# Optimization experiments

Measured on AMD Instinct MI355X. Metric: run time of the kernel, lower is better.

## Reference

```python
import jax, jax.numpy as jnp
import numpy as np

B, T, D, H = 8, 1024, 768, 12
HD = D // H  # 64

def setup_inputs() -> dict:
    key = jax.random.key(0)
    ks = jax.random.split(key, 3)
    x = jax.random.normal(ks[0], (B, T, D), dtype=jnp.float32)
    Wqkv = jax.random.normal(ks[1], (D, 3 * D), dtype=jnp.float32) * (1.0 / np.sqrt(D))
    bqkv = jnp.zeros((3 * D,), dtype=jnp.float32)
    Wproj = jax.random.normal(ks[2], (D, D), dtype=jnp.float32) * (1.0 / np.sqrt(D))
    bproj = jnp.zeros((D,), dtype=jnp.float32)
    return {"x": x, "Wqkv": Wqkv, "bqkv": bqkv, "Wproj": Wproj, "bproj": bproj}

def reference(x, Wqkv, bqkv, Wproj, bproj):
    b, t, d = x.shape
    qkv = x @ Wqkv + bqkv                      # [B,T,3D]
    q, k, v = jnp.split(qkv, 3, axis=-1)
    # [B,T,D] -> [B,H,T,hd]
    q = q.reshape(b, t, H, HD).transpose(0, 2, 1, 3)
    k = k.reshape(b, t, H, HD).transpose(0, 2, 1, 3)
    v = v.reshape(b, t, H, HD).transpose(0, 2, 1, 3)
    scale = 1.0 / np.sqrt(HD)
    att = jnp.einsum('bhqd,bhkd->bhqk', q, k) * scale  # [B,H,T,T]
    causal = jnp.tril(jnp.ones((t, t), dtype=bool))
    att = jnp.where(causal[None, None], att, jnp.float32(-jnp.inf))
    att = jax.nn.softmax(att, axis=-1)
    out = jnp.einsum('bhqk,bhkd->bhqd', att, v)        # [B,H,T,hd]
    out = out.transpose(0, 2, 1, 3).reshape(b, t, d)
    return out @ Wproj + bproj
```

## Files before the change

### kernel.cpp

```cpp
#include <hip/hip_runtime.h>

#define Bn 8
#define Tn 1024
#define Dn 768
#define Hn 12
#define HDn 64
#define D3 (3 * Dn)

typedef float f32x4 __attribute__((ext_vector_type(4)));
typedef short bf16x8 __attribute__((ext_vector_type(8)));
typedef unsigned short u16;

#define SM_SCALE 0.18033688011112042f

__device__ __forceinline__ u16 f2b(float f) {
    unsigned u = __builtin_bit_cast(unsigned, f);
    u += 0x7fffu + ((u >> 16) & 1u);
    return (u16)(u >> 16);
}

__device__ __forceinline__ unsigned cvt_pk_bf16(float lo, float hi) {
    unsigned r;
    asm("v_cvt_pk_bf16_f32 %0, %1, %2" : "=v"(r) : "v"(lo), "v"(hi));
    return r;
}

__device__ __forceinline__ void async_lds16(void* lds, const void* g) {
    __builtin_amdgcn_global_load_lds(
        (const __attribute__((address_space(1))) unsigned int*)g,
        (__attribute__((address_space(3))) unsigned int*)lds, 16, 0, 0);
}

__global__ __launch_bounds__(256)
void conv_bf16_kernel(const float* __restrict__ in, u16* __restrict__ out, int n)
{
    int i = (blockIdx.x * 256 + threadIdx.x) * 4;
    if (i >= n) return;
    float4 v = *(const float4*)&in[i];
    union { u16 u[4]; uint2 p; } r;
    r.u[0] = f2b(v.x); r.u[1] = f2b(v.y); r.u[2] = f2b(v.z); r.u[3] = f2b(v.w);
    *(uint2*)&out[i] = r.p;
}

__global__ __launch_bounds__(256)
void transpose_bf16_kernel(const float* __restrict__ W, u16* __restrict__ WT,
                           int K, int N)
{
    __shared__ float Ls[64][65];
    const int bk = blockIdx.y * 64, bn = blockIdx.x * 64;
    const int r  = threadIdx.x >> 2;
    const int c0 = (threadIdx.x & 3) * 16;
    #pragma unroll
    for (int i = 0; i < 4; ++i) {
        float4 v = *(const float4*)&W[(size_t)(bk + r) * N + bn + c0 + i * 4];
        Ls[r][c0 + i * 4 + 0] = v.x;
        Ls[r][c0 + i * 4 + 1] = v.y;
        Ls[r][c0 + i * 4 + 2] = v.z;
        Ls[r][c0 + i * 4 + 3] = v.w;
    }
    __syncthreads();
    #pragma unroll
    for (int i = 0; i < 16; ++i) {
        WT[(size_t)(bn + r) * K + bk + c0 + i] = f2b(Ls[c0 + i][r]);
    }
}

template <int MODE>
__global__ __launch_bounds__(256)
void gemm_mfma_kernel(const u16* __restrict__ A, const u16* __restrict__ BT,
                      const float* __restrict__ bias, void* __restrict__ Cout,
                      u16* __restrict__ VTout, int M, int N, int K)
{
    __shared__ u16 As[2][128 * 32];
    __shared__ u16 Bs[2][128 * 32];
    const int tid  = threadIdx.x;
    const int w    = tid >> 6;
    const int lane = tid & 63;
    const int li   = lane & 15;
    const int g    = lane >> 4;
    const int wm   = w >> 1, wn = w & 1;

    const int fid = blockIdx.x;
    const int wg  = (fid & 7) * ((int)gridDim.x >> 3) + (fid >> 3);
    const int nbx = N / 128;
    const int bm  = (wg / nbx) * 128;
    const int bn  = (wg % nbx) * 128;

#define GSTAGE(k0s, buf_) do {                                                 \
        _Pragma("unroll")                                                      \
        for (int i_ = 0; i_ < 2; ++i_) {                                       \
            const int L_  = i_ * 256 + tid;                                    \
            const int rp_ = L_ >> 3;                                           \
            const int u_  = (L_ & 7) ^ (rp_ & 7);                              \
            const int row_ = rp_ * 2 + (u_ >> 2);                              \
            const int gc_  = u_ & 3;                                           \
            async_lds16(&As[buf_][(i_ * 256 + w * 64) * 8],                    \
                        &A[(size_t)(bm + row_) * K + (k0s) + gc_ * 8]);        \
            async_lds16(&Bs[buf_][(i_ * 256 + w * 64) * 8],                    \
                        &BT[(size_t)(bn + row_) * K + (k0s) + gc_ * 8]);       \
        }                                                                      \
    } while (0)

    f32x4 acc[4][4];
    #pragma unroll
    for (int i = 0; i < 4; ++i)
        #pragma unroll
        for (int j = 0; j < 4; ++j)
            acc[i][j] = (f32x4){0.f, 0.f, 0.f, 0.f};

    GSTAGE(0, 0);
    __syncthreads();

    const int nk = K / 32;
    for (int kt = 0; kt < nk; ++kt) {
        const int cur = kt & 1;
        if (kt + 1 < nk) GSTAGE((kt + 1) * 32, cur ^ 1);

        bf16x8 af[4], bfr[4];
        #pragma unroll
        for (int fm = 0; fm < 4; ++fm) {
            const int row = wm * 64 + fm * 16 + li;
            const int rp  = row >> 1;
            const int s   = (((row & 1) << 2) | g) ^ (rp & 7);
            af[fm] = *(const bf16x8*)&As[cur][rp * 64 + s * 8];
        }
        #pragma unroll
        for (int fn = 0; fn < 4; ++fn) {
            const int row = wn * 64 + fn * 16 + li;
            const int rp  = row >> 1;
            const int s   = (((row & 1) << 2) | g) ^ (rp & 7);
            bfr[fn] = *(const bf16x8*)&Bs[cur][rp * 64 + s * 8];
        }
        __builtin_amdgcn_s_setprio(1);
        #pragma unroll
        for (int fm = 0; fm < 4; ++fm)
            #pragma unroll
            for (int fn = 0; fn < 4; ++fn)
                acc[fm][fn] = __builtin_amdgcn_mfma_f32_16x16x32_bf16(
                    af[fm], bfr[fn], acc[fm][fn], 0, 0, 0);
        __builtin_amdgcn_s_setprio(0);

        __syncthreads();
    }
#undef GSTAGE

    if (MODE == 1 && bn >= 2 * Dn) {
        #pragma unroll
        for (int fm = 0; fm < 4; ++fm) {
            const int t0g = bm + wm * 64 + fm * 16 + g * 4;
            const int bb = t0g >> 10, tt = t0g & 1023;
            #pragma unroll
            for (int fn = 0; fn < 4; ++fn) {
                const int ncol = bn + wn * 64 + fn * 16 + li;
                const float bs = bias[ncol];
                const int cv = ncol - 2 * Dn;
                const int hv = cv >> 6, dv = cv & 63;
                union { u16 u[4]; uint2 p; } r;
                #pragma unroll
                for (int reg = 0; reg < 4; ++reg)
                    r.u[reg] = f2b(acc[fm][fn][reg] + bs);
                *(uint2*)&VTout[(((size_t)bb * Hn + hv) * HDn + dv) * Tn + tt] = r.p;
            }
        }
    } else {
        #pragma unroll
        for (int fm = 0; fm < 4; ++fm) {
            #pragma unroll
            for (int reg = 0; reg < 4; ++reg) {
                const size_t row = (size_t)(bm + wm * 64 + fm * 16 + g * 4 + reg);
                #pragma unroll
                for (int fn = 0; fn < 4; ++fn) {
                    const int col = bn + wn * 64 + fn * 16 + li;
                    const float v = acc[fm][fn][reg] + bias[col];
                    if (MODE == 1) ((u16*)Cout)[row * N + col] = f2b(v);
                    else           ((float*)Cout)[row * N + col] = v;
                }
            }
        }
    }
}

__global__ __launch_bounds__(256, 3)
void attn_mfma_kernel(const u16* __restrict__ qkvb, const u16* __restrict__ VT,
                      u16* __restrict__ attnb)
{
    __shared__ u16 Ks[2][64 * 64];
    __shared__ u16 Vs[2][64 * 64];
    __shared__ u16 Pb[4][32 * 64];

    const int tid  = threadIdx.x;
    const int w    = tid >> 6;
    const int lane = tid & 63;
    const int li   = lane & 15;
    const int g    = lane >> 4;

    const int fid = blockIdx.x;
    const int xcd = fid & 7, j = fid >> 3;
    const int bh  = xcd + 8 * (j % 12);
    const int qt  = 7 - (j / 12);
    const int b   = bh / 12, h = bh % 12;

    const int q0   = qt * 128;
    const int wrow = q0 + w * 32;
    const size_t rowbase = (size_t)b * Tn;
    const u16* vbase = VT + (size_t)bh * HDn * Tn;
    const u16* kbase = &qkvb[rowbase * D3 + Dn + h * HDn];

#define STAGE(kt_, buf_) do {                                                  \
        const int k0s = (kt_) * 64;                                            \
        _Pragma("unroll")                                                      \
        for (int i_ = 0; i_ < 2; ++i_) {                                       \
            const int L_   = i_ * 256 + tid;                                   \
            const int row_ = L_ >> 3;                                          \
            const int gp_  = (L_ & 7) ^ (row_ & 7);                            \
            async_lds16(&Ks[buf_][(i_ * 256 + w * 64) * 8],                    \
                        &kbase[(size_t)(k0s + row_) * D3 + gp_ * 8]);          \
            async_lds16(&Vs[buf_][(i_ * 256 + w * 64) * 8],                    \
                        &vbase[(size_t)row_ * Tn + k0s + gp_ * 8]);            \
        }                                                                      \
    } while (0)

    STAGE(0, 0);

    bf16x8 qf[2][2];
    #pragma unroll
    for (int rh = 0; rh < 2; ++rh)
        #pragma unroll
        for (int kc = 0; kc < 2; ++kc)
            qf[rh][kc] = *(const bf16x8*)&qkvb[
                (rowbase + wrow + rh * 16 + li) * D3 + h * HDn + kc * 32 + g * 8];

    f32x4 of[2][4];
    float m_run[2], l_run[2];
    #pragma unroll
    for (int rh = 0; rh < 2; ++rh) {
        #pragma unroll
        for (int nf = 0; nf < 4; ++nf) of[rh][nf] = (f32x4){0.f, 0.f, 0.f, 0.f};
        m_run[rh] = -1e30f;
        l_run[rh] = 0.f;
    }

    const int nkt   = (q0 >> 6) + 2;
    const int myend = wrow >> 6;

    __syncthreads();

    for (int kt = 0; kt < nkt; ++kt) {
        const int cur = kt & 1;
        if (kt + 1 < nkt) STAGE(kt + 1, cur ^ 1);

        if (kt <= myend) {
            const int k0 = kt * 64;
            const bool maskit = (kt == myend);

            f32x4 st[2][4];
            #pragma unroll
            for (int rh = 0; rh < 2; ++rh)
                #pragma unroll
                for (int nf = 0; nf < 4; ++nf) st[rh][nf] = (f32x4){0.f, 0.f, 0.f, 0.f};
            __builtin_amdgcn_s_setprio(1);
            #pragma unroll
            for (int kc = 0; kc < 2; ++kc)
                #pragma unroll
                for (int nf = 0; nf < 4; ++nf) {
                    const bf16x8 kf = *(const bf16x8*)&Ks[cur][
                        (nf * 16 + li) * 64 + ((kc * 32 + g * 8) ^ ((li & 7) * 8))];
                    st[0][nf] = __builtin_amdgcn_mfma_f32_16x16x32_bf16(kf, qf[0][kc], st[0][nf], 0, 0, 0);
                    st[1][nf] = __builtin_amdgcn_mfma_f32_16x16x32_bf16(kf, qf[1][kc], st[1][nf], 0, 0, 0);
                }
            __builtin_amdgcn_s_setprio(0);

            #pragma unroll
            for (int rh = 0; rh < 2; ++rh) {
                if (maskit) {
                    const int qg = wrow + rh * 16 + li;
                    #pragma unroll
                    for (int nf = 0; nf < 4; ++nf)
                        #pragma unroll
                        for (int reg = 0; reg < 4; ++reg)
                            if (k0 + nf * 16 + g * 4 + reg > qg) st[rh][nf][reg] = -1e30f;
                }

                float mt = st[rh][0][0];
                #pragma unroll
                for (int nf = 0; nf < 4; ++nf)
                    #pragma unroll
                    for (int reg = 0; reg < 4; ++reg)
                        mt = fmaxf(mt, st[rh][nf][reg]);
                mt = fmaxf(mt, __shfl_xor(mt, 16, 64));
                mt = fmaxf(mt, __shfl_xor(mt, 32, 64));
                const float mts = mt * SM_SCALE;

                const float mold = m_run[rh];
                if (!__all(mts <= mold + 8.0f)) {
                    const float mnew = fmaxf(mold, mts);
                    const float resc = exp2f(mold - mnew);
                    m_run[rh] = mnew;
                    l_run[rh] *= resc;
                    float rs[4];
                    #pragma unroll
                    for (int reg = 0; reg < 4; ++reg)
                        rs[reg] = __shfl(resc, g * 4 + reg, 64);
                    #pragma unroll
                    for (int nf = 0; nf < 4; ++nf)
                        #pragma unroll
                        for (int reg = 0; reg < 4; ++reg)
                            of[rh][nf][reg] *= rs[reg];
                }

                const float mcur = m_run[rh];
                float ls = 0.f;
                u16* pb = &Pb[w][(rh * 16 + li) * 64];
                #pragma unroll
                for (int nf = 0; nf < 4; ++nf) {
                    const float p0 = exp2f(fmaf(st[rh][nf][0], SM_SCALE, -mcur));
                    const float p1 = exp2f(fmaf(st[rh][nf][1], SM_SCALE, -mcur));
                    const float p2 = exp2f(fmaf(st[rh][nf][2], SM_SCALE, -mcur));
                    const float p3 = exp2f(fmaf(st[rh][nf][3], SM_SCALE, -mcur));
                    ls += (p0 + p1) + (p2 + p3);
                    uint2 pk;
                    pk.x = cvt_pk_bf16(p0, p1);
                    pk.y = cvt_pk_bf16(p2, p3);
                    *(uint2*)&pb[(nf * 16 + g * 4) ^ ((li & 7) << 3)] = pk;
                }
                ls += __shfl_xor(ls, 16, 64);
                ls += __shfl_xor(ls, 32, 64);
                l_run[rh] += ls;
            }

            #pragma unroll
            for (int kc = 0; kc < 2; ++kc) {
                const int pcol = (kc * 32 + g * 8) ^ ((li & 7) << 3);
                const bf16x8 pf0 = *(const bf16x8*)&Pb[w][li * 64 + pcol];
                const bf16x8 pf1 = *(const bf16x8*)&Pb[w][(16 + li) * 64 + pcol];
                __builtin_amdgcn_s_setprio(1);
                #pragma unroll
                for (int nf = 0; nf < 4; ++nf) {
                    const bf16x8 vf = *(const bf16x8*)&Vs[cur][
                        (nf * 16 + li) * 64 + ((kc * 32 + g * 8) ^ ((li & 7) * 8))];
                    of[0][nf] = __builtin_amdgcn_mfma_f32_16x16x32_bf16(pf0, vf, of[0][nf], 0, 0, 0);
                    of[1][nf] = __builtin_amdgcn_mfma_f32_16x16x32_bf16(pf1, vf, of[1][nf], 0, 0, 0);
                }
                __builtin_amdgcn_s_setprio(0);
            }
        }

        __syncthreads();
    }
#undef STAGE

    #pragma unroll
    for (int rh = 0; rh < 2; ++rh) {
        const float inv = 1.0f / l_run[rh];
        float rs[4];
        #pragma unroll
        for (int reg = 0; reg < 4; ++reg)
            rs[reg] = __shfl(inv, g * 4 + reg, 64);
        #pragma unroll
        for (int reg = 0; reg < 4; ++reg) {
            const size_t row = rowbase + wrow + rh * 16 + g * 4 + reg;
            #pragma unroll
            for (int nf = 0; nf < 4; ++nf)
                attnb[row * Dn + h * HDn + nf * 16 + li] = f2b(of[rh][nf][reg] * rs[reg]);
        }
    }
}

extern "C" void kernel_launch(void* const* d_in, const int* in_sizes, int n_in,
                              void* d_out, int out_size, void* d_ws, size_t ws_size,
                              hipStream_t stream) {
    const float* x     = (const float*)d_in[0];
    const float* Wqkv  = (const float*)d_in[1];
    const float* bqkv  = (const float*)d_in[2];
    const float* Wproj = (const float*)d_in[3];
    const float* bproj = (const float*)d_in[4];
    float* out = (float*)d_out;

    const int M = Bn * Tn;

    char* ws = (char*)d_ws;
    u16* qkvb   = (u16*)ws;  ws += (size_t)M * D3 * 2;
    u16* xb     = (u16*)ws;  ws += (size_t)M * Dn * 2;
    u16* attnb  = (u16*)ws;  ws += (size_t)M * Dn * 2;
    u16* VT     = (u16*)ws;  ws += (size_t)Bn * Hn * HDn * Tn * 2;
    u16* WqkvT  = (u16*)ws;  ws += (size_t)D3 * Dn * 2;
    u16* WprojT = (u16*)ws;

    conv_bf16_kernel<<<(M * Dn / 4 + 255) / 256, 256, 0, stream>>>(x, xb, M * Dn);
    {
        dim3 gq(D3 / 64, Dn / 64);
        transpose_bf16_kernel<<<gq, 256, 0, stream>>>(Wqkv, WqkvT, Dn, D3);
        dim3 gp(Dn / 64, Dn / 64);
        transpose_bf16_kernel<<<gp, 256, 0, stream>>>(Wproj, WprojT, Dn, Dn);
    }
    {
        const int nwg = (M / 128) * (D3 / 128);
        gemm_mfma_kernel<1><<<nwg, 256, 0, stream>>>(xb, WqkvT, bqkv, qkvb, VT, M, D3, Dn);
    }
    attn_mfma_kernel<<<768, 256, 0, stream>>>(qkvb, VT, attnb);
    {
        const int nwg = (M / 128) * (Dn / 128);
        gemm_mfma_kernel<0><<<nwg, 256, 0, stream>>>(attnb, WprojT, bproj, out, nullptr, M, Dn, Dn);
    }
}
```

Baseline: 120.5 us.

## Double GEMM K-tile to 64 with new swizzle, merge weight transposes, widen conversion

The MFMA GEMM now stages 64-wide K tiles, with a new XOR swizzle on a row-major 64-element LDS layout, and runs two 32-wide MFMA sub-steps per tile. This halves the number of barriers and loop iterations per GEMM. The two weight transpose launches are merged into one 3D-grid launch, and the fp32-to-bf16 conversion now processes 8 elements per thread. LDS use per block doubles to 64 KB, which may lower occupancy.

```diff
diff --git a/kernel.cpp b/kernel.cpp
--- a/kernel.cpp
+++ b/kernel.cpp
@@ -34,18 +34,27 @@
 __global__ __launch_bounds__(256)
 void conv_bf16_kernel(const float* __restrict__ in, u16* __restrict__ out, int n)
 {
-    int i = (blockIdx.x * 256 + threadIdx.x) * 4;
+    int i = (blockIdx.x * 256 + threadIdx.x) * 8;
     if (i >= n) return;
-    float4 v = *(const float4*)&in[i];
-    union { u16 u[4]; uint2 p; } r;
-    r.u[0] = f2b(v.x); r.u[1] = f2b(v.y); r.u[2] = f2b(v.z); r.u[3] = f2b(v.w);
-    *(uint2*)&out[i] = r.p;
+    float4 v0 = *(const float4*)&in[i];
+    float4 v1 = *(const float4*)&in[i + 4];
+    union { u16 u[8]; uint4 p; } r;
+    r.u[0] = f2b(v0.x); r.u[1] = f2b(v0.y); r.u[2] = f2b(v0.z); r.u[3] = f2b(v0.w);
+    r.u[4] = f2b(v1.x); r.u[5] = f2b(v1.y); r.u[6] = f2b(v1.z); r.u[7] = f2b(v1.w);
+    *(uint4*)&out[i] = r.p;
 }
 
 __global__ __launch_bounds__(256)
-void transpose_bf16_kernel(const float* __restrict__ W, u16* __restrict__ WT,
-                           int K, int N)
+void transpose2_bf16_kernel(const float* __restrict__ Wq, u16* __restrict__ WqT,
+                            const float* __restrict__ Wp, u16* __restrict__ WpT)
 {
+    const int z = blockIdx.z;
+    if (z == 1 && blockIdx.x >= Dn / 64) return;
+    const float* W  = z ? Wp : Wq;
+    u16* WT         = z ? WpT : WqT;
+    const int N     = z ? Dn : D3;
+    const int K     = Dn;
+
     __shared__ float Ls[64][65];
     const int bk = blockIdx.y * 64, bn = blockIdx.x * 64;
     const int r  = threadIdx.x >> 2;
@@ -67,12 +76,12 @@
 
 template <int MODE>
 __global__ __launch_bounds__(256)
-void gemm_mfma_kernel(const u16* __restrict__ A, const u16* __restrict__ BT,
+void gemm_bk64_kernel(const u16* __restrict__ A, const u16* __restrict__ BT,
                       const float* __restrict__ bias, void* __restrict__ Cout,
                       u16* __restrict__ VTout, int M, int N, int K)
 {
-    __shared__ u16 As[2][128 * 32];
-    __shared__ u16 Bs[2][128 * 32];
+    __shared__ u16 As[2][128 * 64];
+    __shared__ u16 Bs[2][128 * 64];
     const int tid  = threadIdx.x;
     const int w    = tid >> 6;
     const int lane = tid & 63;
@@ -86,18 +95,16 @@
     const int bm  = (wg / nbx) * 128;
     const int bn  = (wg % nbx) * 128;
 
-#define GSTAGE(k0s, buf_) do {                                                 \
+#define GSTAGE64(k0s, buf_) do {                                               \
         _Pragma("unroll")                                                      \
-        for (int i_ = 0; i_ < 2; ++i_) {                                       \
-            const int L_  = i_ * 256 + tid;                                    \
-            const int rp_ = L_ >> 3;                                           \
-            const int u_  = (L_ & 7) ^ (rp_ & 7);                              \
-            const int row_ = rp_ * 2 + (u_ >> 2);                              \
-            const int gc_  = u_ & 3;                                           \
+        for (int i_ = 0; i_ < 4; ++i_) {                                       \
+            const int L_   = i_ * 256 + tid;                                   \
+            const int row_ = L_ >> 3;                                          \
+            const int gp_  = (L_ & 7) ^ (row_ & 7);                            \
             async_lds16(&As[buf_][(i_ * 256 + w * 64) * 8],                    \
-                        &A[(size_t)(bm + row_) * K + (k0s) + gc_ * 8]);        \
+                        &A[(size_t)(bm + row_) * K + (k0s) + gp_ * 8]);        \
             async_lds16(&Bs[buf_][(i_ * 256 + w * 64) * 8],                    \
-                        &BT[(size_t)(bn + row_) * K + (k0s) + gc_ * 8]);       \
+                        &BT[(size_t)(bn + row_) * K + (k0s) + gp_ * 8]);       \
         }                                                                      \
     } while (0)
 
@@ -108,41 +115,42 @@
         for (int j = 0; j < 4; ++j)
             acc[i][j] = (f32x4){0.f, 0.f, 0.f, 0.f};
 
-    GSTAGE(0, 0);
+    GSTAGE64(0, 0);
     __syncthreads();
 
-    const int nk = K / 32;
+    const int nk = K / 64;
     for (int kt = 0; kt < nk; ++kt) {
         const int cur = kt & 1;
-        if (kt + 1 < nk) GSTAGE((kt + 1) * 32, cur ^ 1);
-
-        bf16x8 af[4], bfr[4];
-        #pragma unroll
-        for (int fm = 0; fm < 4; ++fm) {
-            const int row = wm * 64 + fm * 16 + li;
-            const int rp  = row >> 1;
-            const int s   = (((row & 1) << 2) | g) ^ (rp & 7);
-            af[fm] = *(const bf16x8*)&As[cur][rp * 64 + s * 8];
+        if (kt + 1 < nk) GSTAGE64((kt + 1) * 64, cur ^ 1);
+
+        #pragma unroll
+        for (int kk = 0; kk < 2; ++kk) {
+            bf16x8 af[4], bfr[4];
+            #pragma unroll
+            for (int fm = 0; fm < 4; ++fm) {
+                const int row = wm * 64 + fm * 16 + li;
+                af[fm] = *(const bf16x8*)&As[cur][
+                    row * 64 + ((kk * 32 + g * 8) ^ ((li & 7) * 8))];
+            }
+            #pragma unroll
+            for (int fn = 0; fn < 4; ++fn) {
+                const int row = wn * 64 + fn * 16 + li;
+                bfr[fn] = *(const bf16x8*)&Bs[cur][
+                    row * 64 + ((kk * 32 + g * 8) ^ ((li & 7) * 8))];
+            }
+            __builtin_amdgcn_s_setprio(1);
+            #pragma unroll
+            for (int fm = 0; fm < 4; ++fm)
+                #pragma unroll
+                for (int fn = 0; fn < 4; ++fn)
+                    acc[fm][fn] = __builtin_amdgcn_mfma_f32_16x16x32_bf16(
+                        af[fm], bfr[fn], acc[fm][fn], 0, 0, 0);
+            __builtin_amdgcn_s_setprio(0);
         }
-        #pragma unroll
-        for (int fn = 0; fn < 4; ++fn) {
-            const int row = wn * 64 + fn * 16 + li;
-            const int rp  = row >> 1;
-            const int s   = (((row & 1) << 2) | g) ^ (rp & 7);
-            bfr[fn] = *(const bf16x8*)&Bs[cur][rp * 64 + s * 8];
-        }
-        __builtin_amdgcn_s_setprio(1);
-        #pragma unroll
-        for (int fm = 0; fm < 4; ++fm)
-            #pragma unroll
-            for (int fn = 0; fn < 4; ++fn)
-                acc[fm][fn] = __builtin_amdgcn_mfma_f32_16x16x32_bf16(
-                    af[fm], bfr[fn], acc[fm][fn], 0, 0, 0);
-        __builtin_amdgcn_s_setprio(0);
 
         __syncthreads();
     }
-#undef GSTAGE
+#undef GSTAGE64
 
     if (MODE == 1 && bn >= 2 * Dn) {
         #pragma unroll
@@ -386,20 +394,20 @@
     u16* WqkvT  = (u16*)ws;  ws += (size_t)D3 * Dn * 2;
     u16* WprojT = (u16*)ws;
 
-    conv_bf16_kernel<<<(M * Dn / 4 + 255) / 256, 256, 0, stream>>>(x, xb, M * Dn);
+    conv_bf16_kernel<<<M * Dn / 8 / 256, 256, 0, stream>>>(x, xb, M * Dn);
     {
-        dim3 gq(D3 / 64, Dn / 64);
-        transpose_bf16_kernel<<<gq, 256, 0, stream>>>(Wqkv, WqkvT, Dn, D3);
-        dim3 gp(Dn / 64, Dn / 64);
-        transpose_bf16_kernel<<<gp, 256, 0, stream>>>(Wproj, WprojT, Dn, Dn);
+        dim3 g(D3 / 64, Dn / 64, 2);
+        transpose2_bf16_kernel<<<g, 256, 0, stream>>>(Wqkv, WqkvT, Wproj, WprojT);
     }
     {
         const int nwg = (M / 128) * (D3 / 128);
-        gemm_mfma_kernel<1><<<nwg, 256, 0, stream>>>(xb, WqkvT, bqkv, qkvb, VT, M, D3, Dn);
+        gemm_bk64_kernel<1><<<nwg, 256, 0, stream>>>(
+            xb, WqkvT, bqkv, qkvb, VT, M, D3, Dn);
     }
     attn_mfma_kernel<<<768, 256, 0, stream>>>(qkvb, VT, attnb);
     {
         const int nwg = (M / 128) * (Dn / 128);
-        gemm_mfma_kernel<0><<<nwg, 256, 0, stream>>>(attnb, WprojT, bproj, out, nullptr, M, Dn, Dn);
-    }
-}
+        gemm_bk64_kernel<0><<<nwg, 256, 0, stream>>>(
+            attnb, WprojT, bproj, out, nullptr, M, Dn, Dn);
+    }
+}
```

Result: faster. 115.1 us (-4.5%).
